# Kernel tuning notes

Hardware: AMD Instinct MI355X
Metric: run time of the kernel (lower is better)

The kernel has to match this reference:

```python
import jax, jax.numpy as jnp
import numpy as np

METRIC = [1, 1, 1, 1, -1]  # Cl(4,1) signature (+,+,+,+,-)


def _cayley_table():
    """32x32x32 geometric-product table for Cl(4,1); exactly one nonzero per (i,j)."""
    T = np.zeros((32, 32, 32), dtype=np.float32)
    for i in range(32):
        for j in range(32):
            k = i ^ j
            sign = 1.0
            bits = [b for b in range(5) if (i >> b) & 1] + [b for b in range(5) if (j >> b) & 1]
            swaps = 0
            for _ in range(len(bits)):
                for idx in range(len(bits) - 1):
                    if bits[idx] > bits[idx + 1]:
                        bits[idx], bits[idx + 1] = bits[idx + 1], bits[idx]
                        swaps += 1
            if swaps % 2 == 1:
                sign = -sign
            common = i & j
            for b in range(5):
                if (common >> b) & 1:
                    sign *= METRIC[b]
            T[i, j, k] = sign
    return T


def _mnorm(v, eps=1e-8):
    # stabilized L2 normalization over the last (blade) axis
    return v / (jnp.linalg.norm(v, axis=-1, keepdims=True) + eps)


def setup_inputs() -> dict:
    key = jax.random.key(0)
    k1, k2, k3, k4, k5 = jax.random.split(key, 5)
    B, T, D = 128, 512, 64
    x = jax.random.randint(k1, (B, T), 0, 4)
    emb = jax.random.normal(k2, (4, 32), dtype=jnp.float32) * 0.1
    emb = emb.at[:, 0].set(1.0)  # torch init: weight[:,0] = 1
    gin = 32 + D * 32
    gate_w = jax.random.normal(k3, (D, gin), dtype=jnp.float32) / np.sqrt(gin)
    gate_b = jnp.ones((D,), dtype=jnp.float32)  # torch init: bias.fill_(1.0)
    w1 = jax.random.normal(k4, (128, D * 32), dtype=jnp.float32) / np.sqrt(D * 32)
    b1 = jnp.zeros((128,), dtype=jnp.float32)
    ln_g = jnp.ones((128,), dtype=jnp.float32)
    ln_b = jnp.zeros((128,), dtype=jnp.float32)
    w2 = jax.random.normal(k5, (2, 128), dtype=jnp.float32) / np.sqrt(128)
    b2 = jnp.zeros((2,), dtype=jnp.float32)
    gp_table = jnp.asarray(_cayley_table())
    return {"x": x, "emb": emb, "gate_w": gate_w, "gate_b": gate_b,
            "w1": w1, "b1": b1, "ln_g": ln_g, "ln_b": ln_b,
            "w2": w2, "b2": b2, "gp_table": gp_table}


def reference(x, emb, gate_w, gate_b, w1, b1, ln_g, ln_b, w2, b2, gp_table):
    B, T = x.shape
    D = gate_b.shape[0]
    r_in = _mnorm(emb[x])  # [B,T,32]
    h0 = jnp.zeros((B, D, 32), dtype=emb.dtype).at[:, :, 0].set(1.0)

    def step(h, r_t):
        # r_t: [B,32], h: [B,D,32]
        gate_in = jnp.concatenate([h.reshape(B, D * 32), r_t], axis=-1)
        g = jax.nn.sigmoid(gate_in @ gate_w.T + gate_b)[..., None]  # [B,D,1]
        h_next = jnp.einsum('bi,bdj,ijk->bdk', r_t, h, gp_table)   # geometric product
        h = _mnorm((1.0 - g) * h + g * h_next)
        return h, None

    h, _ = jax.lax.scan(step, h0, jnp.swapaxes(r_in, 0, 1))
    z = h.reshape(B, D * 32) @ w1.T + b1
    mu = jnp.mean(z, axis=-1, keepdims=True)
    var = jnp.var(z, axis=-1, keepdims=True)
    z = (z - mu) / jnp.sqrt(var + 1e-5) * ln_g + ln_b  # LayerNorm(128)
    return jax.nn.relu(z) @ w2.T + b2  # [B,2]
```

## Files before the change

kernel.cpp:

```cpp
#include <hip/hip_runtime.h>
#include <hip/hip_fp16.h>

typedef unsigned int u32;
typedef _Float16 h2f __attribute__((ext_vector_type(2)));

#define BB 128
#define TT 512
#define DD 64
#define NBL 32
#define GIN 2080

template <int CTRL>
__device__ __forceinline__ float dpp_mov_f(float x) {
  return __builtin_bit_cast(
      float, __builtin_amdgcn_update_dpp(0, __builtin_bit_cast(int, x), CTRL,
                                         0xF, 0xF, true));
}
template <int CTRL>
__device__ __forceinline__ float dpp_add_f(float x) {
  return x + dpp_mov_f<CTRL>(x);
}
__device__ __forceinline__ float swz_add16(float x) {
  return x + __builtin_bit_cast(float, __builtin_amdgcn_ds_swizzle(
                                           __builtin_bit_cast(int, x), 0x401F));
}

__device__ inline int gp_negbit(int i, int j) {
  int sw = 0;
#pragma unroll
  for (int b = 0; b < 5; ++b)
    if ((j >> b) & 1) sw += __popc(i >> (b + 1));
  return (sw ^ ((i & j) >> 4)) & 1;
}

__device__ inline float fdot2f(u32 a, u32 b, float acc) {
#if __has_builtin(__builtin_amdgcn_fdot2)
  return __builtin_amdgcn_fdot2(__builtin_bit_cast(h2f, a),
                                __builtin_bit_cast(h2f, b), acc, false);
#else
  h2f av = __builtin_bit_cast(h2f, a), bv = __builtin_bit_cast(h2f, b);
  return acc + (float)av.x * (float)bv.x + (float)av.y * (float)bv.y;
#endif
}

__device__ inline u32 pkf16(float a, float b) {
  return __builtin_bit_cast(u32, __builtin_amdgcn_cvt_pkrtz(a, b));
}

__global__ __launch_bounds__(512, 2) void versor_main(
    const int* __restrict__ x, const float* __restrict__ emb,
    const float* __restrict__ gate_w, const float* __restrict__ gate_b,
    float* __restrict__ ws_h) {
  __shared__ float rn[4][NBL];
  __shared__ __align__(16) float rnq[4][8][4];
  __shared__ float rc[4][DD];
  __shared__ int x_lds[TT];
  __shared__ __align__(16) float h32[2][DD][36];
  __shared__ __align__(16) u32 h16t[2][16][68];

  const int b = blockIdx.x;
  const int tid = threadIdx.x;
  const int w = tid >> 6;
  const int l = tid & 63;
  const int rl = l >> 3;
  const int d = (w << 3) + rl;
  const int c = l & 7;
  const int r2g = l >> 5;
  const int s = l & 31;

  if (tid < 4) {
    float v[NBL];
    float sum = 0.f;
    for (int i = 0; i < NBL; ++i) { v[i] = emb[tid * NBL + i]; sum += v[i] * v[i]; }
    float sc = 1.f / (sqrtf(sum) + 1e-8f);
    for (int i = 0; i < NBL; ++i) rn[tid][i] = v[i] * sc;
    for (int q = 0; q < 8; ++q)
      for (int j = 0; j < 4; ++j) rnq[tid][q][j] = v[q + 8 * j] * sc;
  }
  if (tid < TT) x_lds[tid] = x[b * TT + tid];
  for (int idx = tid; idx < DD * 36; idx += 512) {
    int dd = idx / 36, jj = idx - dd * 36;
    h32[0][dd][jj] = (jj == 0) ? 1.f : 0.f;
  }
  for (int idx = tid; idx < 16 * 68; idx += 512) {
    int m = idx / 68, dd = idx - m * 68;
    h16t[0][m][dd] = (m == 0 && dd < 64) ? 0x00003C00u : 0u;
  }
  __syncthreads();

  if (tid < 256) {
    int e = tid >> 6, row = tid & 63;
    float sum = 0.f;
    for (int i = 0; i < NBL; ++i) sum += gate_w[row * GIN + 2048 + i] * rn[e][i];
    rc[e][row] = sum;
  }

  u32 gw[4][32];
#pragma unroll
  for (int rr = 0; rr < 4; ++rr) {
    const int row = (w << 3) + (r2g << 2) + rr;
    const float* wp = gate_w + row * GIN;
#pragma unroll
    for (int m = 0; m < 32; ++m) {
      int Dd = 32 * s + m;
      int pair = Dd >> 6, dd = Dd & 63;
      int col = dd * 32 + 2 * pair;
      gw[rr][m] = pkf16(wp[col], wp[col + 1]);
    }
  }
  const float gb = gate_b[d];

  u32 sb[NBL];
#pragma unroll
  for (int i = 0; i < NBL; ++i) sb[i] = gp_negbit(i, i ^ c) ? 0x80000000u : 0u;
  __syncthreads();

  for (int t = 0; t < TT; ++t) {
    const int p = t & 1;
    const int pn = p ^ 1;
    const int xi = x_lds[t];

    const u32* Hb = &h16t[p][s >> 1][(s & 1) << 5];
    float a0 = 0.f, a1 = 0.f, a2 = 0.f, a3 = 0.f;
#pragma unroll
    for (int jq = 0; jq < 8; ++jq) {
      uint4 hv = *(const uint4*)(Hb + (jq << 2));
      a0 = fdot2f(gw[0][4 * jq + 0], hv.x, a0);
      a0 = fdot2f(gw[0][4 * jq + 1], hv.y, a0);
      a0 = fdot2f(gw[0][4 * jq + 2], hv.z, a0);
      a0 = fdot2f(gw[0][4 * jq + 3], hv.w, a0);
      a1 = fdot2f(gw[1][4 * jq + 0], hv.x, a1);
      a1 = fdot2f(gw[1][4 * jq + 1], hv.y, a1);
      a1 = fdot2f(gw[1][4 * jq + 2], hv.z, a1);
      a1 = fdot2f(gw[1][4 * jq + 3], hv.w, a1);
      a2 = fdot2f(gw[2][4 * jq + 0], hv.x, a2);
      a2 = fdot2f(gw[2][4 * jq + 1], hv.y, a2);
      a2 = fdot2f(gw[2][4 * jq + 2], hv.z, a2);
      a2 = fdot2f(gw[2][4 * jq + 3], hv.w, a2);
      a3 = fdot2f(gw[3][4 * jq + 0], hv.x, a3);
      a3 = fdot2f(gw[3][4 * jq + 1], hv.y, a3);
      a3 = fdot2f(gw[3][4 * jq + 2], hv.z, a3);
      a3 = fdot2f(gw[3][4 * jq + 3], hv.w, a3);
    }
    a0 = dpp_add_f<0xB1>(a0); a0 = dpp_add_f<0x4E>(a0);
    a0 = dpp_add_f<0x141>(a0); a0 = dpp_add_f<0x140>(a0); a0 = swz_add16(a0);
    a1 = dpp_add_f<0xB1>(a1); a1 = dpp_add_f<0x4E>(a1);
    a1 = dpp_add_f<0x141>(a1); a1 = dpp_add_f<0x140>(a1); a1 = swz_add16(a1);
    a2 = dpp_add_f<0xB1>(a2); a2 = dpp_add_f<0x4E>(a2);
    a2 = dpp_add_f<0x141>(a2); a2 = dpp_add_f<0x140>(a2); a2 = swz_add16(a2);
    a3 = dpp_add_f<0xB1>(a3); a3 = dpp_add_f<0x4E>(a3);
    a3 = dpp_add_f<0x141>(a3); a3 = dpp_add_f<0x140>(a3); a3 = swz_add16(a3);
    const int jsel = rl & 3;
    float zv = (jsel == 0) ? a0 : (jsel == 1) ? a1 : (jsel == 2) ? a2 : a3;
    float zg = zv + rc[xi][d] + gb;
    float g = 1.f / (1.f + exp2f(-1.44269504f * zg));

    float4 hq[8];
#pragma unroll
    for (int q = 0; q < 8; ++q)
      hq[q] = *(const float4*)&h32[p][d][(q ^ c) << 2];

    float b0 = 0.f, b1_ = 0.f, b2_ = 0.f, b3_ = 0.f;
#pragma unroll
    for (int q = 0; q < 8; ++q) {
      float4 rv = *(const float4*)&rnq[xi][q][0];
      float t0 = __builtin_bit_cast(float, __builtin_bit_cast(u32, rv.x) ^ sb[q]);
      float t1 = __builtin_bit_cast(float, __builtin_bit_cast(u32, rv.y) ^ sb[q + 8]);
      float t2 = __builtin_bit_cast(float, __builtin_bit_cast(u32, rv.z) ^ sb[q + 16]);
      float t3 = __builtin_bit_cast(float, __builtin_bit_cast(u32, rv.w) ^ sb[q + 24]);
      b0 = fmaf(t0, hq[q].x, b0);
      b1_ = fmaf(t0, hq[q].y, b1_);
      b2_ = fmaf(t0, hq[q].z, b2_);
      b3_ = fmaf(t0, hq[q].w, b3_);
      b0 = fmaf(t1, hq[q].y, b0);
      b1_ = fmaf(t1, hq[q].x, b1_);
      b2_ = fmaf(t1, hq[q].w, b2_);
      b3_ = fmaf(t1, hq[q].z, b3_);
      b0 = fmaf(t2, hq[q].z, b0);
      b1_ = fmaf(-t2, hq[q].w, b1_);
      b2_ = fmaf(-t2, hq[q].x, b2_);
      b3_ = fmaf(t2, hq[q].y, b3_);
      b0 = fmaf(t3, hq[q].w, b0);
      b1_ = fmaf(-t3, hq[q].z, b1_);
      b2_ = fmaf(-t3, hq[q].y, b2_);
      b3_ = fmaf(t3, hq[q].x, b3_);
    }

    float u0 = fmaf(g, b0 - hq[0].x, hq[0].x);
    float u1 = fmaf(g, b1_ - hq[0].y, hq[0].y);
    float u2 = fmaf(g, b2_ - hq[0].z, hq[0].z);
    float u3 = fmaf(g, b3_ - hq[0].w, hq[0].w);
    float sq = u0 * u0 + u1 * u1 + u2 * u2 + u3 * u3;
    sq = dpp_add_f<0xB1>(sq);
    sq = dpp_add_f<0x4E>(sq);
    sq = dpp_add_f<0x141>(sq);
    float sc = 1.f / (sqrtf(sq) + 1e-8f);
    u0 *= sc; u1 *= sc; u2 *= sc; u3 *= sc;

    *(float4*)&h32[pn][d][c << 2] = make_float4(u0, u1, u2, u3);

    float v0 = dpp_mov_f<0xB1>(u0);
    float v1 = dpp_mov_f<0xB1>(u1);
    float v2 = dpp_mov_f<0xB1>(u2);
    float v3 = dpp_mov_f<0xB1>(u3);
    if (!(l & 1)) {
      h16t[pn][(c) >> 1][d] = pkf16(u0, v0);
      h16t[pn][(c + 8) >> 1][d] = pkf16(u1, v1);
      h16t[pn][(c + 16) >> 1][d] = pkf16(u2, v2);
      h16t[pn][(c + 24) >> 1][d] = pkf16(u3, v3);
    }
    __syncthreads();
  }

  for (int idx = tid; idx < DD * NBL; idx += 512) {
    int dd = idx >> 5, blade = idx & 31;
    int o = blade & 7, j = blade >> 3;
    ws_h[b * 2048 + idx] = h32[0][dd][4 * o + j];
  }
}

__global__ __launch_bounds__(512) void versor_head(
    const float* __restrict__ ws_h, const float* __restrict__ w1,
    const float* __restrict__ b1, const float* __restrict__ ln_g,
    const float* __restrict__ ln_b, const float* __restrict__ w2,
    const float* __restrict__ b2, float* __restrict__ out) {
  __shared__ __align__(16) float hs[4][2048];
  __shared__ float red[8][2];
  const int bb = blockIdx.x;
  const int tid = threadIdx.x;
  for (int idx = tid; idx < 8192; idx += 512)
    ((float*)hs)[idx] = ws_h[bb * 8192 + idx];
  __syncthreads();

  const int r = tid & 127;
  const int bs = tid >> 7;
  float acc = b1[r];
  const float4* w4 = (const float4*)(w1 + r * 2048);
  const float4* h4 = (const float4*)&hs[bs][0];
#pragma unroll 4
  for (int k = 0; k < 512; ++k) {
    float4 wv = w4[k];
    float4 hv = h4[k];
    acc = fmaf(hv.x, wv.x, acc);
    acc = fmaf(hv.y, wv.y, acc);
    acc = fmaf(hv.z, wv.z, acc);
    acc = fmaf(hv.w, wv.w, acc);
  }

  float s1 = acc, s2 = acc * acc;
#pragma unroll
  for (int off = 1; off <= 32; off <<= 1) {
    s1 += __shfl_xor(s1, off, 64);
    s2 += __shfl_xor(s2, off, 64);
  }
  const int wv = tid >> 6;
  if ((tid & 63) == 0) { red[wv][0] = s1; red[wv][1] = s2; }
  __syncthreads();
  float t1 = red[2 * bs][0] + red[2 * bs + 1][0];
  float t2 = red[2 * bs][1] + red[2 * bs + 1][1];
  float mu = t1 * (1.f / 128.f);
  float var = t2 * (1.f / 128.f) - mu * mu;
  float z = (acc - mu) * rsqrtf(var + 1e-5f) * ln_g[r] + ln_b[r];
  z = fmaxf(z, 0.f);
  __syncthreads();

  float p0 = z * w2[r], p1 = z * w2[128 + r];
#pragma unroll
  for (int off = 1; off <= 32; off <<= 1) {
    p0 += __shfl_xor(p0, off, 64);
    p1 += __shfl_xor(p1, off, 64);
  }
  if ((tid & 63) == 0) { red[wv][0] = p0; red[wv][1] = p1; }
  __syncthreads();
  if ((tid & 127) == 0) {
    int bo = (bb * 4 + bs) * 2;
    out[bo + 0] = red[2 * bs][0] + red[2 * bs + 1][0] + b2[0];
    out[bo + 1] = red[2 * bs][1] + red[2 * bs + 1][1] + b2[1];
  }
}

extern "C" void kernel_launch(void* const* d_in, const int* in_sizes, int n_in,
                              void* d_out, int out_size, void* d_ws,
                              size_t ws_size, hipStream_t stream) {
  (void)in_sizes; (void)n_in; (void)out_size; (void)ws_size;
  const int* x = (const int*)d_in[0];
  const float* emb = (const float*)d_in[1];
  const float* gate_w = (const float*)d_in[2];
  const float* gate_b = (const float*)d_in[3];
  const float* w1 = (const float*)d_in[4];
  const float* b1 = (const float*)d_in[5];
  const float* ln_g = (const float*)d_in[6];
  const float* ln_b = (const float*)d_in[7];
  const float* w2 = (const float*)d_in[8];
  const float* b2 = (const float*)d_in[9];
  float* out = (float*)d_out;
  float* ws_h = (float*)d_ws;

  versor_main<<<dim3(BB), dim3(512), 0, stream>>>(x, emb, gate_w, gate_b, ws_h);
  versor_head<<<dim3(32), dim3(512), 0, stream>>>(ws_h, w1, b1, ln_g, ln_b, w2,
                                                  b2, out);
}
```

Baseline: 992.2 us.

## Keep fp32 hidden state in registers with DPP butterflies instead of LDS

```diff
diff --git a/kernel.cpp b/kernel.cpp
--- a/kernel.cpp
+++ b/kernel.cpp
@@ -23,6 +23,13 @@
 __device__ __forceinline__ float swz_add16(float x) {
   return x + __builtin_bit_cast(float, __builtin_amdgcn_ds_swizzle(
                                            __builtin_bit_cast(int, x), 0x401F));
+}
+__device__ __forceinline__ float swz4(float x) {
+  return __builtin_bit_cast(float, __builtin_amdgcn_ds_swizzle(
+                                       __builtin_bit_cast(int, x), 0x101F));
+}
+__device__ __forceinline__ float xorf(float a, u32 m) {
+  return __builtin_bit_cast(float, __builtin_bit_cast(u32, a) ^ m);
 }
 
 __device__ inline int gp_negbit(int i, int j) {
@@ -52,10 +59,8 @@
     const float* __restrict__ gate_w, const float* __restrict__ gate_b,
     float* __restrict__ ws_h) {
   __shared__ float rn[4][NBL];
-  __shared__ __align__(16) float rnq[4][8][4];
+  __shared__ float inv_lds[4];
   __shared__ float rc[4][DD];
-  __shared__ int x_lds[TT];
-  __shared__ __align__(16) float h32[2][DD][36];
   __shared__ __align__(16) u32 h16t[2][16][68];
 
   const int b = blockIdx.x;
@@ -71,16 +76,13 @@
   if (tid < 4) {
     float v[NBL];
     float sum = 0.f;
-    for (int i = 0; i < NBL; ++i) { v[i] = emb[tid * NBL + i]; sum += v[i] * v[i]; }
+    for (int i = 0; i < NBL; ++i) {
+      v[i] = emb[tid * NBL + i];
+      sum += v[i] * v[i];
+    }
     float sc = 1.f / (sqrtf(sum) + 1e-8f);
+    inv_lds[tid] = sc;
     for (int i = 0; i < NBL; ++i) rn[tid][i] = v[i] * sc;
-    for (int q = 0; q < 8; ++q)
-      for (int j = 0; j < 4; ++j) rnq[tid][q][j] = v[q + 8 * j] * sc;
-  }
-  if (tid < TT) x_lds[tid] = x[b * TT + tid];
-  for (int idx = tid; idx < DD * 36; idx += 512) {
-    int dd = idx / 36, jj = idx - dd * 36;
-    h32[0][dd][jj] = (jj == 0) ? 1.f : 0.f;
   }
   for (int idx = tid; idx < 16 * 68; idx += 512) {
     int m = idx / 68, dd = idx - m * 68;
@@ -115,10 +117,36 @@
   for (int i = 0; i < NBL; ++i) sb[i] = gp_negbit(i, i ^ c) ? 0x80000000u : 0u;
   __syncthreads();
 
-  for (int t = 0; t < TT; ++t) {
-    const int p = t & 1;
+  float rcv[4], invv[4];
+#pragma unroll
+  for (int e = 0; e < 4; ++e) {
+    rcv[e] = rc[e][d] + gb;
+    invv[e] = inv_lds[e];
+  }
+
+  float u0 = (c == 0) ? 1.f : 0.f, u1 = 0.f, u2 = 0.f, u3 = 0.f;
+  float4 hq[8];
+  auto bfly = [&]() {
+    hq[0] = make_float4(u0, u1, u2, u3);
+    hq[1] = make_float4(dpp_mov_f<0xB1>(u0), dpp_mov_f<0xB1>(u1),
+                        dpp_mov_f<0xB1>(u2), dpp_mov_f<0xB1>(u3));
+    hq[2] = make_float4(dpp_mov_f<0x4E>(u0), dpp_mov_f<0x4E>(u1),
+                        dpp_mov_f<0x4E>(u2), dpp_mov_f<0x4E>(u3));
+    hq[3] = make_float4(dpp_mov_f<0x1B>(u0), dpp_mov_f<0x1B>(u1),
+                        dpp_mov_f<0x1B>(u2), dpp_mov_f<0x1B>(u3));
+    float s0 = swz4(u0), s1 = swz4(u1), s2 = swz4(u2), s3 = swz4(u3);
+    hq[4] = make_float4(s0, s1, s2, s3);
+    hq[5] = make_float4(dpp_mov_f<0xB1>(s0), dpp_mov_f<0xB1>(s1),
+                        dpp_mov_f<0xB1>(s2), dpp_mov_f<0xB1>(s3));
+    hq[6] = make_float4(dpp_mov_f<0x4E>(s0), dpp_mov_f<0x4E>(s1),
+                        dpp_mov_f<0x4E>(s2), dpp_mov_f<0x4E>(s3));
+    hq[7] = make_float4(dpp_mov_f<0x1B>(s0), dpp_mov_f<0x1B>(s1),
+                        dpp_mov_f<0x1B>(s2), dpp_mov_f<0x1B>(s3));
+  };
+  bfly();
+
+  auto step = [&](int p, int xi, const float (&rnr)[NBL]) {
     const int pn = p ^ 1;
-    const int xi = x_lds[t];
 
     const u32* Hb = &h16t[p][s >> 1][(s & 1) << 5];
     float a0 = 0.f, a1 = 0.f, a2 = 0.f, a3 = 0.f;
@@ -152,22 +180,20 @@
     a3 = dpp_add_f<0x141>(a3); a3 = dpp_add_f<0x140>(a3); a3 = swz_add16(a3);
     const int jsel = rl & 3;
     float zv = (jsel == 0) ? a0 : (jsel == 1) ? a1 : (jsel == 2) ? a2 : a3;
-    float zg = zv + rc[xi][d] + gb;
+    float rcsel = (xi == 0) ? rcv[0] : (xi == 1) ? rcv[1]
+                  : (xi == 2) ? rcv[2] : rcv[3];
+    float invsel = (xi == 0) ? invv[0] : (xi == 1) ? invv[1]
+                   : (xi == 2) ? invv[2] : invv[3];
+    float zg = zv + rcsel;
     float g = 1.f / (1.f + exp2f(-1.44269504f * zg));
 
-    float4 hq[8];
-#pragma unroll
-    for (int q = 0; q < 8; ++q)
-      hq[q] = *(const float4*)&h32[p][d][(q ^ c) << 2];
-
     float b0 = 0.f, b1_ = 0.f, b2_ = 0.f, b3_ = 0.f;
 #pragma unroll
     for (int q = 0; q < 8; ++q) {
-      float4 rv = *(const float4*)&rnq[xi][q][0];
-      float t0 = __builtin_bit_cast(float, __builtin_bit_cast(u32, rv.x) ^ sb[q]);
-      float t1 = __builtin_bit_cast(float, __builtin_bit_cast(u32, rv.y) ^ sb[q + 8]);
-      float t2 = __builtin_bit_cast(float, __builtin_bit_cast(u32, rv.z) ^ sb[q + 16]);
-      float t3 = __builtin_bit_cast(float, __builtin_bit_cast(u32, rv.w) ^ sb[q + 24]);
+      float t0 = xorf(rnr[q], sb[q]);
+      float t1 = xorf(rnr[q + 8], sb[q + 8]);
+      float t2 = xorf(rnr[q + 16], sb[q + 16]);
+      float t3 = xorf(rnr[q + 24], sb[q + 24]);
       b0 = fmaf(t0, hq[q].x, b0);
       b1_ = fmaf(t0, hq[q].y, b1_);
       b2_ = fmaf(t0, hq[q].z, b2_);
@@ -186,18 +212,18 @@
       b3_ = fmaf(t3, hq[q].x, b3_);
     }
 
-    float u0 = fmaf(g, b0 - hq[0].x, hq[0].x);
-    float u1 = fmaf(g, b1_ - hq[0].y, hq[0].y);
-    float u2 = fmaf(g, b2_ - hq[0].z, hq[0].z);
-    float u3 = fmaf(g, b3_ - hq[0].w, hq[0].w);
+    float gi = g * invsel;
+    float om = 1.f - g;
+    u0 = fmaf(gi, b0, om * hq[0].x);
+    u1 = fmaf(gi, b1_, om * hq[0].y);
+    u2 = fmaf(gi, b2_, om * hq[0].z);
+    u3 = fmaf(gi, b3_, om * hq[0].w);
     float sq = u0 * u0 + u1 * u1 + u2 * u2 + u3 * u3;
     sq = dpp_add_f<0xB1>(sq);
     sq = dpp_add_f<0x4E>(sq);
     sq = dpp_add_f<0x141>(sq);
     float sc = 1.f / (sqrtf(sq) + 1e-8f);
     u0 *= sc; u1 *= sc; u2 *= sc; u3 *= sc;
-
-    *(float4*)&h32[pn][d][c << 2] = make_float4(u0, u1, u2, u3);
 
     float v0 = dpp_mov_f<0xB1>(u0);
     float v1 = dpp_mov_f<0xB1>(u1);
@@ -209,73 +235,90 @@
       h16t[pn][(c + 16) >> 1][d] = pkf16(u2, v2);
       h16t[pn][(c + 24) >> 1][d] = pkf16(u3, v3);
     }
+    bfly();
     __syncthreads();
-  }
-
-  for (int idx = tid; idx < DD * NBL; idx += 512) {
-    int dd = idx >> 5, blade = idx & 31;
-    int o = blade & 7, j = blade >> 3;
-    ws_h[b * 2048 + idx] = h32[0][dd][4 * o + j];
-  }
-}
-
-__global__ __launch_bounds__(512) void versor_head(
+  };
+
+  const int* xg = x + b * TT;
+  int xiA = xg[0];
+  int xiB = xg[1];
+  float rnA[NBL], rnB[NBL];
+#pragma unroll
+  for (int i = 0; i < NBL; ++i) rnA[i] = emb[xiA * NBL + i];
+
+  for (int t = 0; t < TT; t += 2) {
+#pragma unroll
+    for (int i = 0; i < NBL; ++i) rnB[i] = emb[xiB * NBL + i];
+    int xiC = xg[(t + 2 < TT) ? t + 2 : 0];
+    step(0, xiA, rnA);
+#pragma unroll
+    for (int i = 0; i < NBL; ++i) rnA[i] = emb[xiC * NBL + i];
+    int xiD = xg[(t + 3 < TT) ? t + 3 : 0];
+    step(1, xiB, rnB);
+    xiA = xiC;
+    xiB = xiD;
+  }
+
+  float* wo = ws_h + b * 2048 + d * 32 + c;
+  wo[0] = u0;
+  wo[8] = u1;
+  wo[16] = u2;
+  wo[24] = u3;
+}
+
+__global__ __launch_bounds__(256) void versor_head(
     const float* __restrict__ ws_h, const float* __restrict__ w1,
     const float* __restrict__ b1, const float* __restrict__ ln_g,
     const float* __restrict__ ln_b, const float* __restrict__ w2,
     const float* __restrict__ b2, float* __restrict__ out) {
-  __shared__ __align__(16) float hs[4][2048];
-  __shared__ float red[8][2];
-  const int bb = blockIdx.x;
-  const int tid = threadIdx.x;
-  for (int idx = tid; idx < 8192; idx += 512)
-    ((float*)hs)[idx] = ws_h[bb * 8192 + idx];
-  __syncthreads();
-
-  const int r = tid & 127;
-  const int bs = tid >> 7;
-  float acc = b1[r];
-  const float4* w4 = (const float4*)(w1 + r * 2048);
-  const float4* h4 = (const float4*)&hs[bs][0];
-#pragma unroll 4
-  for (int k = 0; k < 512; ++k) {
-    float4 wv = w4[k];
-    float4 hv = h4[k];
-    acc = fmaf(hv.x, wv.x, acc);
-    acc = fmaf(hv.y, wv.y, acc);
-    acc = fmaf(hv.z, wv.z, acc);
-    acc = fmaf(hv.w, wv.w, acc);
-  }
-
+  __shared__ __align__(16) float hs[2048];
+  __shared__ float red[4][2];
+  const int bctx = blockIdx.x, tid = threadIdx.x;
+  {
+    const float4* src = (const float4*)(ws_h + bctx * 2048);
+    float4* dst = (float4*)hs;
+    for (int i = tid; i < 512; i += 256) dst[i] = src[i];
+  }
+  __syncthreads();
+  const int r = tid >> 1, half = tid & 1, wv = tid >> 6;
+  float acc = half ? 0.f : b1[r];
+  const float4* w4 = (const float4*)(w1 + r * 2048 + half * 1024);
+  const float4* h4 = (const float4*)(hs + half * 1024);
+#pragma unroll 8
+  for (int k = 0; k < 256; ++k) {
+    float4 a = w4[k], hv = h4[k];
+    acc = fmaf(a.x, hv.x, acc);
+    acc = fmaf(a.y, hv.y, acc);
+    acc = fmaf(a.z, hv.z, acc);
+    acc = fmaf(a.w, hv.w, acc);
+  }
+  acc += __shfl_xor(acc, 1, 64);
   float s1 = acc, s2 = acc * acc;
 #pragma unroll
-  for (int off = 1; off <= 32; off <<= 1) {
+  for (int off = 2; off <= 32; off <<= 1) {
     s1 += __shfl_xor(s1, off, 64);
     s2 += __shfl_xor(s2, off, 64);
   }
-  const int wv = tid >> 6;
   if ((tid & 63) == 0) { red[wv][0] = s1; red[wv][1] = s2; }
   __syncthreads();
-  float t1 = red[2 * bs][0] + red[2 * bs + 1][0];
-  float t2 = red[2 * bs][1] + red[2 * bs + 1][1];
-  float mu = t1 * (1.f / 128.f);
-  float var = t2 * (1.f / 128.f) - mu * mu;
+  float tot1 = red[0][0] + red[1][0] + red[2][0] + red[3][0];
+  float tot2 = red[0][1] + red[1][1] + red[2][1] + red[3][1];
+  float mu = tot1 * (1.f / 128.f);
+  float var = tot2 * (1.f / 128.f) - mu * mu;
   float z = (acc - mu) * rsqrtf(var + 1e-5f) * ln_g[r] + ln_b[r];
   z = fmaxf(z, 0.f);
   __syncthreads();
-
   float p0 = z * w2[r], p1 = z * w2[128 + r];
 #pragma unroll
-  for (int off = 1; off <= 32; off <<= 1) {
+  for (int off = 2; off <= 32; off <<= 1) {
     p0 += __shfl_xor(p0, off, 64);
     p1 += __shfl_xor(p1, off, 64);
   }
   if ((tid & 63) == 0) { red[wv][0] = p0; red[wv][1] = p1; }
   __syncthreads();
-  if ((tid & 127) == 0) {
-    int bo = (bb * 4 + bs) * 2;
-    out[bo + 0] = red[2 * bs][0] + red[2 * bs + 1][0] + b2[0];
-    out[bo + 1] = red[2 * bs][1] + red[2 * bs + 1][1] + b2[1];
+  if (tid == 0) {
+    out[bctx * 2 + 0] = red[0][0] + red[1][0] + red[2][0] + red[3][0] + b2[0];
+    out[bctx * 2 + 1] = red[0][1] + red[1][1] + red[2][1] + red[3][1] + b2[1];
   }
 }
 
@@ -297,6 +340,6 @@
   float* ws_h = (float*)d_ws;
 
   versor_main<<<dim3(BB), dim3(512), 0, stream>>>(x, emb, gate_w, gate_b, ws_h);
-  versor_head<<<dim3(32), dim3(512), 0, stream>>>(ws_h, w1, b1, ln_g, ln_b, w2,
+  versor_head<<<dim3(BB), dim3(256), 0, stream>>>(ws_h, w1, b1, ln_g, ln_b, w2,
                                                   b2, out);
 }
```

Result: slower. 1.021 ms (+2.9%).
